# Performance work log

Hardware: AMD Instinct MI355X
Metric: run time of the kernel (lower is better)

Reference implementation:

```python
import jax, jax.numpy as jnp
import numpy as np

B, C, N = 2, 1024, 80
D = 3 * C + 2  # 3074 token dim
DFF = 2048     # torch TransformerEncoderLayer default dim_feedforward
HW = 224
REFINE = 3
EPS = 1e-5


def _layernorm(x, g, b):
    m = jnp.mean(x, axis=-1, keepdims=True)
    v = jnp.mean((x - m) ** 2, axis=-1, keepdims=True)
    return g * (x - m) / jnp.sqrt(v + EPS) + b


def _pos_encoding(seq_len, dim):
    pos = jnp.arange(seq_len, dtype=jnp.float32)[:, None]
    div = jnp.exp(jnp.arange(0, dim, 2, dtype=jnp.float32) * (-np.log(10000.0) / dim))
    pe = jnp.zeros((seq_len, dim), dtype=jnp.float32)
    pe = pe.at[:, 0::2].set(jnp.sin(pos * div)).at[:, 1::2].set(jnp.cos(pos * div))
    return pe


def _forward(pre_f, curr_f, first_f, ln_g, ln_b, ipw, ipb, opw, opb,
             n1g, n1b, l1w, l1b, l2w, l2b, n2g, n2b, ow, ob,
             prev_b, first_b):
    # --- vectorized find_best_shift: batched circular L1 correlation ---
    idx = (jnp.arange(N)[None, :] - jnp.arange(N)[:, None]) % N  # [shift, pos]
    rolled = first_b[:, idx]                                     # [B, N, N, 2]
    dist = jnp.abs(prev_b[:, None] - rolled).sum(axis=(-1, -2))  # [B, N]
    best = jnp.argmin(dist, axis=1)                              # first min, like torch loop
    roll_idx = (jnp.arange(N)[None, :] - best[:, None]) % N      # [B, N]
    first_b = jax.vmap(lambda fb, ri: fb[ri])(first_b, roll_idx)

    # --- bilinear upsample to 224x224 (F.interpolate, align_corners=False) ---
    up = lambda f: jax.image.resize(f, (f.shape[0], f.shape[1], HW, HW), method='bilinear')
    pre_up, curr_up, first_up = up(pre_f), up(curr_f), up(first_f)

    # --- vectorized get_bou_features: [B,N,C] gather ---
    gather = jax.vmap(lambda f, b: f[:, b[:, 0], b[:, 1]].T)
    pre_q = gather(pre_up, prev_b)      # [B, N, C]
    first_q = gather(first_up, first_b)  # [B, N, C]

    pe = _pos_encoding(N, D)
    curr = prev_b.astype(jnp.float32)
    scale = 1.0 / jnp.sqrt(jnp.float32(D))
    results = []
    for _ in range(REFINE):
        bf = gather(curr_up, curr.astype(jnp.int32))          # [B, N, C]
        tokens = jnp.concatenate([pre_q, bf, curr, first_q], axis=-1)  # [B, N, D]
        tokens = _layernorm(tokens, ln_g, ln_b)
        tokens = tokens + pe[None]
        # --- TransformerEncoderLayer (post-norm, nhead=1, relu, eval/no dropout) ---
        qkv = tokens @ ipw.T + ipb
        q, k, v = jnp.split(qkv, 3, axis=-1)
        attn = jax.nn.softmax(jnp.einsum('bqd,bkd->bqk', q, k) * scale, axis=-1)
        a = jnp.einsum('bqk,bkd->bqd', attn, v) @ opw.T + opb
        x = _layernorm(tokens + a, n1g, n1b)
        ff = jax.nn.relu(x @ l1w.T + l1b) @ l2w.T + l2b
        x = _layernorm(x + ff, n2g, n2b)
        out = x @ ow.T + ob                                   # [B, N, 1026]
        curr = jnp.clip(curr + out[..., C:], 0.0, 223.0)
        pre_q = pre_q + out[..., :C]
        results.append(curr)
    return jnp.stack(results)  # [REFINE, B, N, 2]


def setup_inputs() -> dict:
    key = jax.random.key(0)
    ks = jax.random.split(key, 12)
    f = lambda i, s: jax.random.normal(ks[i], s, dtype=jnp.float32)
    w = lambda i, s: 0.02 * jax.random.normal(ks[i], s, dtype=jnp.float32)
    return {
        'pre_img_features': f(0, (B, C, 14, 14)),
        'curr_img_features': f(1, (B, C, 14, 14)),
        'first_img_features': f(2, (B, C, 14, 14)),
        'previous_boundary': jax.random.randint(ks[3], (B, N, 2), 0, HW),
        'first_boundary': jax.random.randint(ks[4], (B, N, 2), 0, HW),
        'ln_g': jnp.ones((D,), jnp.float32), 'ln_b': jnp.zeros((D,), jnp.float32),
        'in_proj_w': w(5, (3 * D, D)), 'in_proj_b': jnp.zeros((3 * D,), jnp.float32),
        'out_proj_w': w(6, (D, D)), 'out_proj_b': jnp.zeros((D,), jnp.float32),
        'norm1_g': jnp.ones((D,), jnp.float32), 'norm1_b': jnp.zeros((D,), jnp.float32),
        'lin1_w': w(7, (DFF, D)), 'lin1_b': jnp.zeros((DFF,), jnp.float32),
        'lin2_w': w(8, (D, DFF)), 'lin2_b': jnp.zeros((D,), jnp.float32),
        'norm2_g': jnp.ones((D,), jnp.float32), 'norm2_b': jnp.zeros((D,), jnp.float32),
        'out_w': w(9, (C + 2, D)), 'out_b': jnp.zeros((C + 2,), jnp.float32),
    }


def reference(pre_img_features, curr_img_features, first_img_features,
              previous_boundary, first_boundary,
              ln_g, ln_b, in_proj_w, in_proj_b, out_proj_w, out_proj_b,
              norm1_g, norm1_b, lin1_w, lin1_b, lin2_w, lin2_b,
              norm2_g, norm2_b, out_w, out_b):
    return _forward(pre_img_features, curr_img_features, first_img_features,
                    ln_g, ln_b, in_proj_w, in_proj_b, out_proj_w, out_proj_b,
                    norm1_g, norm1_b, lin1_w, lin1_b, lin2_w, lin2_b,
                    norm2_g, norm2_b, out_w, out_b,
                    previous_boundary, first_boundary)
```

## Files before the change

### kernel.cpp

```cpp
#include <hip/hip_runtime.h>
#include <math.h>

#define B_    2
#define C_    1024
#define N_    80
#define D_    3074
#define DFF_  2048
#define OD_   1026
#define QKV_  9222
#define M_    160
#define EPS_  1e-5f
#define KPD_  3104

typedef __attribute__((ext_vector_type(8))) short bf16x8;
typedef __attribute__((ext_vector_type(4))) float f32x4;

__device__ inline short f2bf(float f) {
    unsigned u = __float_as_uint(f);
    u += 0x7fffu + ((u >> 16) & 1u);
    return (short)(u >> 16);
}

__device__ inline float wave_sum(float v) {
#pragma unroll
    for (int off = 32; off > 0; off >>= 1) v += __shfl_down(v, off, 64);
    return v;
}

__device__ inline float wave_max(float v) {
#pragma unroll
    for (int off = 32; off > 0; off >>= 1) v = fmaxf(v, __shfl_down(v, off, 64));
    return v;
}

__device__ inline void block_reduce_2(float& s, float& s2, float* red) {
    int tid = threadIdx.x;
    int lane = tid & 63, wid = tid >> 6;
    s = wave_sum(s);
    s2 = wave_sum(s2);
    if (lane == 0) { red[wid] = s; red[4 + wid] = s2; }
    __syncthreads();
    if (tid == 0) {
        red[8] = red[0] + red[1] + red[2] + red[3];
        red[9] = red[4] + red[5] + red[6] + red[7];
    }
    __syncthreads();
    s = red[8]; s2 = red[9];
}

__device__ inline void bilin_setup(int p, int& i0, int& i1, float& t) {
    float s = (p + 0.5f) * 0.0625f - 0.5f;
    s = fminf(fmaxf(s, 0.0f), 13.0f);
    i0 = (int)s;
    t = s - (float)i0;
    i1 = min(i0 + 1, 13);
}

__device__ inline float bilin_tap(const float* f, int y0, int y1, float ty,
                                  int x0, int x1, float tx) {
    float a = f[y0 * 14 + x0], b = f[y0 * 14 + x1];
    float c = f[y1 * 14 + x0], d = f[y1 * 14 + x1];
    return (1.f - ty) * ((1.f - tx) * a + tx * b) + ty * ((1.f - tx) * c + tx * d);
}

__global__ __launch_bounds__(128) void align_kernel(const int* __restrict__ prev_b,
                                                    const int* __restrict__ first_b,
                                                    int* __restrict__ fb_al) {
    int b = blockIdx.x;
    int tid = threadIdx.x;
    __shared__ int dist[N_];
    __shared__ int bestIdx;
    if (tid < N_) {
        int s = 0;
        for (int j = 0; j < N_; ++j) {
            int src = (j - tid) % N_;
            if (src < 0) src += N_;
            int dy = prev_b[(b * N_ + j) * 2] - first_b[(b * N_ + src) * 2];
            int dx = prev_b[(b * N_ + j) * 2 + 1] - first_b[(b * N_ + src) * 2 + 1];
            s += abs(dy) + abs(dx);
        }
        dist[tid] = s;
    }
    __syncthreads();
    if (tid == 0) {
        int best = 0, bd = dist[0];
        for (int i = 1; i < N_; ++i)
            if (dist[i] < bd) { bd = dist[i]; best = i; }
        bestIdx = best;
    }
    __syncthreads();
    if (tid < N_) {
        int src = (tid - bestIdx) % N_;
        if (src < 0) src += N_;
        fb_al[(b * N_ + tid) * 2]     = first_b[(b * N_ + src) * 2];
        fb_al[(b * N_ + tid) * 2 + 1] = first_b[(b * N_ + src) * 2 + 1];
    }
}

__global__ __launch_bounds__(256) void gather_init_kernel(
        const float* __restrict__ pre_f, const float* __restrict__ first_f,
        const int* __restrict__ prev_b, const int* __restrict__ fb_al,
        float* __restrict__ pre_q, float* __restrict__ first_q,
        float* __restrict__ curr) {
    int m = blockIdx.x;
    int b = m / N_;
    int tid = threadIdx.x;
    int py = prev_b[m * 2], px = prev_b[m * 2 + 1];
    int fy = fb_al[m * 2], fx = fb_al[m * 2 + 1];
    int py0, py1, px0, px1, fy0, fy1, fx0, fx1;
    float pty, ptx, fty, ftx;
    bilin_setup(py, py0, py1, pty);
    bilin_setup(px, px0, px1, ptx);
    bilin_setup(fy, fy0, fy1, fty);
    bilin_setup(fx, fx0, fx1, ftx);
    for (int c = tid; c < C_; c += 256) {
        const float* fp = pre_f + (size_t)(b * C_ + c) * 196;
        const float* ff = first_f + (size_t)(b * C_ + c) * 196;
        pre_q[(size_t)m * C_ + c]   = bilin_tap(fp, py0, py1, pty, px0, px1, ptx);
        first_q[(size_t)m * C_ + c] = bilin_tap(ff, fy0, fy1, fty, fx0, fx1, ftx);
    }
    if (tid < 2) curr[m * 2 + tid] = (float)prev_b[m * 2 + tid];
}

__global__ __launch_bounds__(256) void tokens_kernel(
        const float* __restrict__ curr_f, const float* __restrict__ pre_q,
        const float* __restrict__ first_q, const float* __restrict__ curr,
        const float* __restrict__ ln_g, const float* __restrict__ ln_b,
        float* __restrict__ tokens, short* __restrict__ tokens_bf) {
    int m = blockIdx.x;
    int b = m / N_;
    int n = m % N_;
    int tid = threadIdx.x;
    __shared__ float bf[C_];
    __shared__ float red[10];

    float cy = curr[m * 2], cx = curr[m * 2 + 1];
    int iy = (int)cy, ix = (int)cx;
    int y0, y1, x0, x1;
    float ty, tx;
    bilin_setup(iy, y0, y1, ty);
    bilin_setup(ix, x0, x1, tx);
    for (int c = tid; c < C_; c += 256) {
        const float* f = curr_f + (size_t)(b * C_ + c) * 196;
        bf[c] = bilin_tap(f, y0, y1, ty, x0, x1, tx);
    }
    __syncthreads();

    float s = 0.f, s2 = 0.f;
    for (int d = tid; d < D_; d += 256) {
        float v;
        if (d < C_)            v = pre_q[(size_t)m * C_ + d];
        else if (d < 2 * C_)   v = bf[d - C_];
        else if (d == 2 * C_)  v = cy;
        else if (d == 2*C_+1)  v = cx;
        else                   v = first_q[(size_t)m * C_ + (d - 2 * C_ - 2)];
        s += v; s2 += v * v;
    }
    block_reduce_2(s, s2, red);
    float mean = s / (float)D_;
    float var = s2 / (float)D_ - mean * mean;
    float inv = rsqrtf(var + EPS_);

    const float negLogDivD = -logf(10000.0f) / (float)D_;
    for (int d = tid; d < KPD_; d += 256) {
        if (d < D_) {
            float v;
            if (d < C_)            v = pre_q[(size_t)m * C_ + d];
            else if (d < 2 * C_)   v = bf[d - C_];
            else if (d == 2 * C_)  v = cy;
            else if (d == 2*C_+1)  v = cx;
            else                   v = first_q[(size_t)m * C_ + (d - 2 * C_ - 2)];
            float ln = ln_g[d] * (v - mean) * inv + ln_b[d];
            int kk = d >> 1;
            float ang = (float)n * expf((float)(2 * kk) * negLogDivD);
            float pe = (d & 1) ? cosf(ang) : sinf(ang);
            float val = ln + pe;
            tokens[(size_t)m * D_ + d] = val;
            tokens_bf[(size_t)m * KPD_ + d] = f2bf(val);
        } else {
            tokens_bf[(size_t)m * KPD_ + d] = 0;
        }
    }
}

__global__ __launch_bounds__(256) void wpack_kernel(const float* __restrict__ w,
                                                    short* __restrict__ o,
                                                    int K, int O, int nch) {
    int s = blockIdx.x;
    int items = nch * 64;
    for (int idx = threadIdx.x; idx < items; idx += 256) {
        int c = idx >> 6, l = idx & 63;
        int col = l & 15, quad = l >> 4;
        int orow = s * 16 + col;
        int k0 = c * 32 + quad * 8;
        bf16x8 v;
        if (orow < O && k0 + 8 <= K) {
            const float* src = w + (size_t)orow * K + k0;
            float2 a = *(const float2*)(src);
            float2 b = *(const float2*)(src + 2);
            float2 cc = *(const float2*)(src + 4);
            float2 d = *(const float2*)(src + 6);
            v[0] = f2bf(a.x);  v[1] = f2bf(a.y);
            v[2] = f2bf(b.x);  v[3] = f2bf(b.y);
            v[4] = f2bf(cc.x); v[5] = f2bf(cc.y);
            v[6] = f2bf(d.x);  v[7] = f2bf(d.y);
        } else {
#pragma unroll
            for (int j = 0; j < 8; ++j) {
                int k = k0 + j;
                v[j] = (orow < O && k < K) ? f2bf(w[(size_t)orow * K + k]) : (short)0;
            }
        }
        *(bf16x8*)(o + ((size_t)s * nch + c) * 512 + l * 8) = v;
    }
}

__global__ __launch_bounds__(256) void gemm_pk(
        const short* __restrict__ A, const short* __restrict__ Wp,
        const float* __restrict__ bias, float* __restrict__ Cout,
        int KpA, int nch, int O) {
    int strip = blockIdx.x;
    int nsk = gridDim.y;
    int mg = blockIdx.z;
    int lane = threadIdx.x & 63, wave = threadIdx.x >> 6;
    int col = lane & 15, quad = lane >> 4;

    int per = (nch + nsk - 1) / nsk;
    int cs = blockIdx.y * per;
    int ce = min(nch, cs + per);
    if (cs >= ce) return;
    int tot = ce - cs;
    int qn = tot >> 2, rmd = tot & 3;
    int c0 = cs + wave * qn + min(wave, rmd);
    int c1 = c0 + qn + (wave < rmd ? 1 : 0);

    const short* wp = Wp + (size_t)strip * nch * 512 + lane * 8;
    const short* ap = A + (size_t)(mg * 80 + col) * KpA + quad * 8;

    f32x4 acc[5];
#pragma unroll
    for (int t = 0; t < 5; ++t)
#pragma unroll
        for (int r = 0; r < 4; ++r) acc[t][r] = 0.f;

    if (c0 < c1) {
        bf16x8 wcur = *(const bf16x8*)(wp + (size_t)c0 * 512);
        for (int c = c0; c < c1; ++c) {
            bf16x8 wnxt = wcur;
            if (c + 1 < c1) wnxt = *(const bf16x8*)(wp + (size_t)(c + 1) * 512);
#pragma unroll
            for (int t = 0; t < 5; ++t) {
                bf16x8 af = *(const bf16x8*)(ap + (size_t)t * 16 * KpA + c * 32);
                acc[t] = __builtin_amdgcn_mfma_f32_16x16x32_bf16(af, wcur, acc[t], 0, 0, 0);
            }
            wcur = wnxt;
        }
    }

    __shared__ f32x4 red[4][5][64];
#pragma unroll
    for (int t = 0; t < 5; ++t) red[wave][t][lane] = acc[t];
    __syncthreads();
    for (int item = threadIdx.x; item < 320; item += 256) {
        int t = item >> 6, l2 = item & 63;
        f32x4 v = red[0][t][l2];
#pragma unroll
        for (int w = 1; w < 4; ++w)
#pragma unroll
            for (int r = 0; r < 4; ++r) v[r] += red[w][t][l2][r];
        int oc = strip * 16 + (l2 & 15);
        if (oc < O) {
            float bv = (blockIdx.y == 0) ? bias[oc] : 0.f;
            int rbase = mg * 80 + t * 16 + (l2 >> 4) * 4;
#pragma unroll
            for (int r = 0; r < 4; ++r) {
                float val = v[r] + bv;
                if (nsk == 1) Cout[(size_t)(rbase + r) * O + oc] = val;
                else atomicAdd(&Cout[(size_t)(rbase + r) * O + oc], val);
            }
        }
    }
}

__global__ __launch_bounds__(256) void gemm_mfma_sk(
        const short* __restrict__ A, const float* __restrict__ Wf,
        const float* __restrict__ bias, float* __restrict__ Cout,
        int K, int KpA, int O, int KC) {
    int kc0 = blockIdx.y * KC;
    if (kc0 >= K) return;
    int kend = min(K, kc0 + KC);

    int lane = threadIdx.x & 63;
    int wave = threadIdx.x >> 6;
    int col  = lane & 15;
    int quad = lane >> 4;
    int o0 = blockIdx.x * 128 + wave * 32 + col;
    int o1 = o0 + 16;
    int oc0 = min(o0, O - 1), oc1 = min(o1, O - 1);

    const float* wrow0 = Wf + (size_t)oc0 * K + quad * 8;
    const float* wrow1 = Wf + (size_t)oc1 * K + quad * 8;
    const short* abase = A + (size_t)col * KpA + quad * 8;

    f32x4 acc0[10], acc1[10];
#pragma unroll
    for (int t = 0; t < 10; ++t)
#pragma unroll
        for (int r = 0; r < 4; ++r) { acc0[t][r] = 0.f; acc1[t][r] = 0.f; }

    int nfull = (kend - kc0) >> 5;
    bf16x8 aCur[10];
    float2 wCur[8];
    if (nfull > 0) {
#pragma unroll
        for (int t = 0; t < 10; ++t)
            aCur[t] = *(const bf16x8*)(abase + (size_t)t * 16 * KpA + kc0);
#pragma unroll
        for (int j = 0; j < 4; ++j) {
            wCur[j]     = *(const float2*)(wrow0 + kc0 + 2 * j);
            wCur[4 + j] = *(const float2*)(wrow1 + kc0 + 2 * j);
        }
    }
    for (int i = 0; i < nfull; ++i) {
        bf16x8 aNxt[10];
        float2 wNxt[8];
        if (i + 1 < nfull) {
            int kn = kc0 + (i + 1) * 32;
#pragma unroll
            for (int t = 0; t < 10; ++t)
                aNxt[t] = *(const bf16x8*)(abase + (size_t)t * 16 * KpA + kn);
#pragma unroll
            for (int j = 0; j < 4; ++j) {
                wNxt[j]     = *(const float2*)(wrow0 + kn + 2 * j);
                wNxt[4 + j] = *(const float2*)(wrow1 + kn + 2 * j);
            }
        }
        bf16x8 b0, b1;
#pragma unroll
        for (int j = 0; j < 4; ++j) {
            b0[2*j] = f2bf(wCur[j].x);     b0[2*j+1] = f2bf(wCur[j].y);
            b1[2*j] = f2bf(wCur[4+j].x);   b1[2*j+1] = f2bf(wCur[4+j].y);
        }
#pragma unroll
        for (int t = 0; t < 10; ++t) {
            acc0[t] = __builtin_amdgcn_mfma_f32_16x16x32_bf16(aCur[t], b0, acc0[t], 0, 0, 0);
            acc1[t] = __builtin_amdgcn_mfma_f32_16x16x32_bf16(aCur[t], b1, acc1[t], 0, 0, 0);
        }
#pragma unroll
        for (int t = 0; t < 10; ++t) aCur[t] = aNxt[t];
#pragma unroll
        for (int j = 0; j < 8; ++j) wCur[j] = wNxt[j];
    }
    int kmain = kc0 + nfull * 32;
    if (kmain < kend) {
        bf16x8 b0, b1;
#pragma unroll
        for (int j = 0; j < 8; ++j) {
            int k = kmain + quad * 8 + j;
            b0[j] = (k < kend) ? f2bf(Wf[(size_t)oc0 * K + k]) : (short)0;
            b1[j] = (k < kend) ? f2bf(Wf[(size_t)oc1 * K + k]) : (short)0;
        }
#pragma unroll
        for (int t = 0; t < 10; ++t) {
            bf16x8 af = *(const bf16x8*)(abase + (size_t)t * 16 * KpA + kmain);
            acc0[t] = __builtin_amdgcn_mfma_f32_16x16x32_bf16(af, b0, acc0[t], 0, 0, 0);
            acc1[t] = __builtin_amdgcn_mfma_f32_16x16x32_bf16(af, b1, acc1[t], 0, 0, 0);
        }
    }
    if (o0 < O) {
        float bv = (blockIdx.y == 0) ? bias[o0] : 0.f;
#pragma unroll
        for (int t = 0; t < 10; ++t)
#pragma unroll
            for (int r = 0; r < 4; ++r)
                atomicAdd(&Cout[(size_t)(t * 16 + quad * 4 + r) * O + o0], acc0[t][r] + bv);
    }
    if (o1 < O) {
        float bv = (blockIdx.y == 0) ? bias[o1] : 0.f;
#pragma unroll
        for (int t = 0; t < 10; ++t)
#pragma unroll
            for (int r = 0; r < 4; ++r)
                atomicAdd(&Cout[(size_t)(t * 16 + quad * 4 + r) * O + o1], acc1[t][r] + bv);
    }
}

__global__ __launch_bounds__(256) void relu_cvt_kernel(const float* __restrict__ in,
                                                       short* __restrict__ out,
                                                       int n) {
    int i = blockIdx.x * 256 + threadIdx.x;
    if (i < n) out[i] = f2bf(fmaxf(in[i], 0.f));
}

__global__ __launch_bounds__(256) void qkv_cvt_kernel(const float* __restrict__ qkv,
                                                      short* __restrict__ q_bf,
                                                      short* __restrict__ k_bf,
                                                      short* __restrict__ v_bf) {
    int m = blockIdx.x;
    int b = m / N_, q = m % N_;
    const float* src = qkv + (size_t)m * QKV_;
    for (int d = threadIdx.x; d < KPD_; d += 256) {
        short qv = (d < D_) ? f2bf(src[d])          : (short)0;
        short kv = (d < D_) ? f2bf(src[D_ + d])     : (short)0;
        short vv = (d < D_) ? f2bf(src[2 * D_ + d]) : (short)0;
        q_bf[(size_t)m * KPD_ + d] = qv;
        k_bf[(size_t)m * KPD_ + d] = kv;
        v_bf[((size_t)b * 96 + q) * KPD_ + d] = vv;
    }
}

__global__ __launch_bounds__(256) void scores_mfma(const short* __restrict__ q_bf,
                                                   const short* __restrict__ k_bf,
                                                   float* __restrict__ sc) {
    int bi = blockIdx.x;
    int b = bi / 25, qt = (bi % 25) / 5, kt = bi % 5;
    int lane = threadIdx.x & 63, wave = threadIdx.x >> 6;
    int col = lane & 15, quad = lane >> 4;
    const short* qbase = q_bf + (size_t)(b * N_ + qt * 16 + col) * KPD_ + quad * 8;
    const short* kbase = k_bf + (size_t)(b * N_ + kt * 16 + col) * KPD_ + quad * 8;
    f32x4 acc;
#pragma unroll
    for (int r = 0; r < 4; ++r) acc[r] = 0.f;
    int c0 = wave * 25, c1 = min(97, c0 + 25);
    for (int c = c0; c < c1; ++c) {
        bf16x8 af = *(const bf16x8*)(qbase + c * 32);
        bf16x8 bf8 = *(const bf16x8*)(kbase + c * 32);
        acc = __builtin_amdgcn_mfma_f32_16x16x32_bf16(af, bf8, acc, 0, 0, 0);
    }
    __shared__ f32x4 red[4][64];
    red[wave][lane] = acc;
    __syncthreads();
    if (threadIdx.x < 64) {
        f32x4 t = red[0][lane];
#pragma unroll
        for (int w = 1; w < 4; ++w)
#pragma unroll
            for (int r = 0; r < 4; ++r) t[r] += red[w][lane][r];
        float scale = rsqrtf((float)D_);
#pragma unroll
        for (int r = 0; r < 4; ++r)
            sc[(size_t)(b * N_ + qt * 16 + quad * 4 + r) * N_ + kt * 16 + col] = t[r] * scale;
    }
}

__global__ __launch_bounds__(256) void softmax_kernel(const float* __restrict__ sc,
                                                      short* __restrict__ p_bf) {
    int m = blockIdx.x * 4 + (threadIdx.x >> 6);
    int lane = threadIdx.x & 63;
    const float* row = sc + (size_t)m * N_;
    float a = row[lane];
    float bv = (lane < 16) ? row[64 + lane] : -1e30f;
    float mx = wave_max(fmaxf(a, bv));
    mx = __shfl(mx, 0, 64);
    float e0 = expf(a - mx);
    float e1 = (lane < 16) ? expf(bv - mx) : 0.f;
    float sum = wave_sum(e0 + e1);
    sum = __shfl(sum, 0, 64);
    float rs = 1.0f / sum;
    p_bf[(size_t)m * 96 + lane] = f2bf(e0 * rs);
    if (lane < 32)
        p_bf[(size_t)m * 96 + 64 + lane] = (lane < 16) ? f2bf(e1 * rs) : (short)0;
}

__global__ __launch_bounds__(256) void av_mfma(const short* __restrict__ p_bf,
                                               const short* __restrict__ v_bf,
                                               short* __restrict__ av_bf) {
    int bi = blockIdx.x;
    int b = bi / 49, g = bi % 49;
    int lane = threadIdx.x & 63, wave = threadIdx.x >> 6;
    int dtile = g * 4 + wave;
    if (dtile >= 194) return;
    int d0 = dtile * 16;
    int col = lane & 15, quad = lane >> 4;
    const short* pbase = p_bf + (size_t)b * N_ * 96 + quad * 8;
    const short* vb = v_bf + (size_t)b * 96 * KPD_ + d0 + col;
    f32x4 acc[5];
#pragma unroll
    for (int t = 0; t < 5; ++t)
#pragma unroll
        for (int r = 0; r < 4; ++r) acc[t][r] = 0.f;
#pragma unroll
    for (int c = 0; c < 3; ++c) {
        bf16x8 bf8;
#pragma unroll
        for (int j = 0; j < 8; ++j)
            bf8[j] = vb[(size_t)(c * 32 + quad * 8 + j) * KPD_];
#pragma unroll
        for (int t = 0; t < 5; ++t) {
            bf16x8 af = *(const bf16x8*)(pbase + (size_t)(t * 16 + col) * 96 + c * 32);
            acc[t] = __builtin_amdgcn_mfma_f32_16x16x32_bf16(af, bf8, acc[t], 0, 0, 0);
        }
    }
#pragma unroll
    for (int t = 0; t < 5; ++t)
#pragma unroll
        for (int r = 0; r < 4; ++r)
            av_bf[(size_t)(b * N_ + t * 16 + quad * 4 + r) * KPD_ + d0 + col] = f2bf(acc[t][r]);
}

template <bool WF32>
__global__ __launch_bounds__(256) void ln_kernel(const float* __restrict__ xin,
                                                 const float* __restrict__ res,
                                                 const float* __restrict__ g,
                                                 const float* __restrict__ bta,
                                                 float* __restrict__ outf,
                                                 short* __restrict__ outb) {
    int m = blockIdx.x;
    int tid = threadIdx.x;
    __shared__ float red[10];
    const float* xr = xin + (size_t)m * D_;
    const float* rr = res + (size_t)m * D_;
    float s = 0.f, s2 = 0.f;
    for (int d = tid; d < D_; d += 256) {
        float v = xr[d] + rr[d];
        s += v; s2 += v * v;
    }
    block_reduce_2(s, s2, red);
    float mean = s / (float)D_;
    float var = s2 / (float)D_ - mean * mean;
    float inv = rsqrtf(var + EPS_);
    for (int d = tid; d < KPD_; d += 256) {
        if (d < D_) {
            float v = xr[d] + rr[d];
            float y = g[d] * (v - mean) * inv + bta[d];
            if (WF32) outf[(size_t)m * D_ + d] = y;
            outb[(size_t)m * KPD_ + d] = f2bf(y);
        } else {
            outb[(size_t)m * KPD_ + d] = 0;
        }
    }
}

__global__ __launch_bounds__(256) void update_kernel(const float* __restrict__ outb,
                                                     float* __restrict__ curr,
                                                     float* __restrict__ pre_q,
                                                     float* __restrict__ results) {
    int m = blockIdx.x;
    int tid = threadIdx.x;
    for (int c = tid; c < C_; c += 256)
        pre_q[(size_t)m * C_ + c] += outb[(size_t)m * OD_ + c];
    if (tid < 2) {
        float nc = curr[m * 2 + tid] + outb[(size_t)m * OD_ + C_ + tid];
        nc = fminf(fmaxf(nc, 0.f), 223.f);
        curr[m * 2 + tid] = nc;
        results[m * 2 + tid] = nc;
    }
}

extern "C" void kernel_launch(void* const* d_in, const int* in_sizes, int n_in,
                              void* d_out, int out_size, void* d_ws, size_t ws_size,
                              hipStream_t stream) {
    const float* pre_f   = (const float*)d_in[0];
    const float* curr_f  = (const float*)d_in[1];
    const float* first_f = (const float*)d_in[2];
    const int*   prev_b  = (const int*)d_in[3];
    const int*   first_b = (const int*)d_in[4];
    const float* ln_g    = (const float*)d_in[5];
    const float* ln_b    = (const float*)d_in[6];
    const float* ipw     = (const float*)d_in[7];
    const float* ipb     = (const float*)d_in[8];
    const float* opw     = (const float*)d_in[9];
    const float* opb     = (const float*)d_in[10];
    const float* n1g     = (const float*)d_in[11];
    const float* n1b     = (const float*)d_in[12];
    const float* l1w     = (const float*)d_in[13];
    const float* l1b     = (const float*)d_in[14];
    const float* l2w     = (const float*)d_in[15];
    const float* l2b     = (const float*)d_in[16];
    const float* n2g     = (const float*)d_in[17];
    const float* n2b     = (const float*)d_in[18];
    const float* ow      = (const float*)d_in[19];
    const float* ob      = (const float*)d_in[20];
    float* outp = (float*)d_out;

    float* wf = (float*)d_ws;
    size_t off = 0;
    int*   fb_al   = (int*)(wf + off); off += 320;
    float* curr    = wf + off;         off += 320;
    float* pre_q   = wf + off;         off += (size_t)M_ * C_;
    float* first_q = wf + off;         off += (size_t)M_ * C_;
    float* tokens  = wf + off;         off += (size_t)M_ * D_;
    float* qkv     = wf + off;         off += (size_t)M_ * QKV_;
    float* aout    = wf + off;         off += (size_t)M_ * D_;
    float* xbuf    = wf + off;         off += (size_t)M_ * D_;
    float* ff1f    = wf + off;         off += (size_t)M_ * DFF_;
    float* ffout   = wf + off;         off += (size_t)M_ * D_;
    float* outb    = wf + off;         off += (size_t)M_ * OD_;
    float* sc      = wf + off;         off += (size_t)M_ * N_;
    short* tokens_bf = (short*)(wf + off); off += (size_t)M_ * KPD_ / 2;
    short* x_bf      = (short*)(wf + off); off += (size_t)M_ * KPD_ / 2;
    short* x2_bf     = (short*)(wf + off); off += (size_t)M_ * KPD_ / 2;
    short* av_bf     = (short*)(wf + off); off += (size_t)M_ * KPD_ / 2;
    short* ff1_bf    = (short*)(wf + off); off += (size_t)M_ * DFF_ / 2;
    short* q_bf      = (short*)(wf + off); off += (size_t)M_ * KPD_ / 2;
    short* k_bf      = (short*)(wf + off); off += (size_t)M_ * KPD_ / 2;
    short* v_bf      = (short*)(wf + off); off += (size_t)B_ * 96 * KPD_ / 2;
    short* p_bf      = (short*)(wf + off); off += (size_t)M_ * 96 / 2;
    short* ipw_pk = (short*)(wf + off); off += (size_t)577 * 97 * 256;
    short* opw_pk = (short*)(wf + off); off += (size_t)193 * 97 * 256;
    short* l1w_pk = (short*)(wf + off); off += (size_t)128 * 97 * 256;
    short* l2w_pk = (short*)(wf + off); off += (size_t)193 * 64 * 256;
    short* ow_pk  = (short*)(wf + off); off += (size_t)65  * 97 * 256;
    bool use_bf = ws_size >= off * sizeof(float);
    (void)in_sizes; (void)n_in; (void)out_size;

    hipLaunchKernelGGL(align_kernel, dim3(B_), dim3(128), 0, stream,
                       prev_b, first_b, fb_al);
    hipLaunchKernelGGL(gather_init_kernel, dim3(M_), dim3(256), 0, stream,
                       pre_f, first_f, prev_b, fb_al, pre_q, first_q, curr);
    hipMemsetAsync(v_bf, 0, (size_t)B_ * 96 * KPD_ * 2, stream);

    if (use_bf) {
        hipLaunchKernelGGL(wpack_kernel, dim3(577), dim3(256), 0, stream, ipw, ipw_pk, D_, QKV_, 97);
        hipLaunchKernelGGL(wpack_kernel, dim3(193), dim3(256), 0, stream, opw, opw_pk, D_, D_, 97);
        hipLaunchKernelGGL(wpack_kernel, dim3(128), dim3(256), 0, stream, l1w, l1w_pk, D_, DFF_, 97);
        hipLaunchKernelGGL(wpack_kernel, dim3(193), dim3(256), 0, stream, l2w, l2w_pk, DFF_, D_, 64);
        hipLaunchKernelGGL(wpack_kernel, dim3(65),  dim3(256), 0, stream, ow, ow_pk, D_, OD_, 97);
    }

    for (int it = 0; it < 3; ++it) {
        if (!use_bf) hipMemsetAsync(qkv, 0, (size_t)M_ * QKV_ * 4, stream);
        hipMemsetAsync(aout,  0, (size_t)M_ * D_   * 4, stream);
        hipMemsetAsync(ff1f,  0, (size_t)M_ * DFF_ * 4, stream);
        hipMemsetAsync(ffout, 0, (size_t)M_ * D_   * 4, stream);
        hipMemsetAsync(outb,  0, (size_t)M_ * OD_  * 4, stream);

        hipLaunchKernelGGL(tokens_kernel, dim3(M_), dim3(256), 0, stream,
                           curr_f, pre_q, first_q, curr, ln_g, ln_b, tokens, tokens_bf);
        if (use_bf)
            hipLaunchKernelGGL(gemm_pk, dim3(577, 1, 2), dim3(256), 0, stream,
                               tokens_bf, ipw_pk, ipb, qkv, KPD_, 97, QKV_);
        else
            hipLaunchKernelGGL(gemm_mfma_sk, dim3(73, 6), dim3(256), 0, stream,
                               tokens_bf, ipw, ipb, qkv, D_, KPD_, QKV_, 544);
        hipLaunchKernelGGL(qkv_cvt_kernel, dim3(M_), dim3(256), 0, stream,
                           qkv, q_bf, k_bf, v_bf);
        hipLaunchKernelGGL(scores_mfma, dim3(50), dim3(256), 0, stream,
                           q_bf, k_bf, sc);
        hipLaunchKernelGGL(softmax_kernel, dim3(40), dim3(256), 0, stream,
                           sc, p_bf);
        hipLaunchKernelGGL(av_mfma, dim3(98), dim3(256), 0, stream,
                           p_bf, v_bf, av_bf);
        if (use_bf)
            hipLaunchKernelGGL(gemm_pk, dim3(193, 2, 2), dim3(256), 0, stream,
                               av_bf, opw_pk, opb, aout, KPD_, 97, D_);
        else
            hipLaunchKernelGGL(gemm_mfma_sk, dim3(25, 10), dim3(256), 0, stream,
                               av_bf, opw, opb, aout, D_, KPD_, D_, 320);
        hipLaunchKernelGGL((ln_kernel<true>), dim3(M_), dim3(256), 0, stream,
                           tokens, aout, n1g, n1b, xbuf, x_bf);
        if (use_bf)
            hipLaunchKernelGGL(gemm_pk, dim3(128, 2, 2), dim3(256), 0, stream,
                               x_bf, l1w_pk, l1b, ff1f, KPD_, 97, DFF_);
        else
            hipLaunchKernelGGL(gemm_mfma_sk, dim3(16, 17), dim3(256), 0, stream,
                               x_bf, l1w, l1b, ff1f, D_, KPD_, DFF_, 192);
        hipLaunchKernelGGL(relu_cvt_kernel, dim3((M_ * DFF_ + 255) / 256), dim3(256), 0, stream,
                           ff1f, ff1_bf, M_ * DFF_);
        if (use_bf)
            hipLaunchKernelGGL(gemm_pk, dim3(193, 2, 2), dim3(256), 0, stream,
                               ff1_bf, l2w_pk, l2b, ffout, DFF_, 64, D_);
        else
            hipLaunchKernelGGL(gemm_mfma_sk, dim3(25, 11), dim3(256), 0, stream,
                               ff1_bf, l2w, l2b, ffout, DFF_, DFF_, D_, 192);
        hipLaunchKernelGGL((ln_kernel<false>), dim3(M_), dim3(256), 0, stream,
                           xbuf, ffout, n2g, n2b, (float*)nullptr, x2_bf);
        if (use_bf)
            hipLaunchKernelGGL(gemm_pk, dim3(65, 4, 2), dim3(256), 0, stream,
                               x2_bf, ow_pk, ob, outb, KPD_, 97, OD_);
        else
            hipLaunchKernelGGL(gemm_mfma_sk, dim3(9, 13), dim3(256), 0, stream,
                               x2_bf, ow, ob, outb, D_, KPD_, OD_, 256);
        hipLaunchKernelGGL(update_kernel, dim3(M_), dim3(256), 0, stream,
                           outb, curr, pre_q, outp + (size_t)it * M_ * 2);
    }
}
```

Measured before the change: 1.040 ms.

## Add split-K LDS double-buffered GEMM writing partials, reduce them in consumer kernels

Adds a gemm_stage kernel that stages the 160-row activation tile in LDS with double buffering and gives each wave several output strips. Each split-K slice writes plain stores into a partial buffer instead of using atomics. The downstream kernels (qkv_cvt, ln, relu_cvt, update) now sum those partials, so the per-iteration memsets and atomic traffic go away. Weight packing is also spread over more blocks. The cost is a large partial buffer and extra read traffic in the reduction kernels, and the new path only runs when the workspace is big enough.

After: 1.134 ms. +9.0%, slower.

```diff
diff --git a/kernel.cpp b/kernel.cpp
--- a/kernel.cpp
+++ b/kernel.cpp
@@ -11,6 +11,12 @@
 #define M_    160
 #define EPS_  1e-5f
 #define KPD_  3104
+
+#define SQKV 6
+#define SOP  14
+#define SFF1 14
+#define SFF2 16
+#define SHD  14
 
 typedef __attribute__((ext_vector_type(8))) short bf16x8;
 typedef __attribute__((ext_vector_type(4))) float f32x4;
@@ -188,7 +194,10 @@
                                                     int K, int O, int nch) {
     int s = blockIdx.x;
     int items = nch * 64;
-    for (int idx = threadIdx.x; idx < items; idx += 256) {
+    int qlen = (items + 3) >> 2;
+    int beg = blockIdx.y * qlen;
+    int end = min(items, beg + qlen);
+    for (int idx = beg + threadIdx.x; idx < end; idx += 256) {
         int c = idx >> 6, l = idx & 63;
         int col = l & 15, quad = l >> 4;
         int orow = s * 16 + col;
@@ -215,6 +224,98 @@
     }
 }
 
+template <int SW>
+__global__ __launch_bounds__(256) void gemm_stage(
+        const short* __restrict__ A, const short* __restrict__ Wp,
+        const float* __restrict__ bias, float* __restrict__ part,
+        int KpA, int nch, int O, int per) {
+    int cs = blockIdx.y * per;
+    int ce = min(nch, cs + per);
+    if (cs >= ce) return;
+    int tid = threadIdx.x;
+    int lane = tid & 63, wave = tid >> 6;
+    int col = lane & 15, quad = lane >> 4;
+    int s0 = (blockIdx.x * 4 + wave) * SW;
+
+    __shared__ short lbuf[2][160 * 32];
+
+    int m0 = tid >> 2, p8 = (tid & 3) * 8;
+    int m1 = (tid + 256) >> 2;
+    int m2 = (tid + 512) >> 2;
+    const short* a0 = A + (size_t)m0 * KpA + p8;
+    const short* a1 = A + (size_t)m1 * KpA + p8;
+    const short* a2 = A + (size_t)m2 * KpA + p8;
+    bf16x8 sr0, sr1, sr2;
+
+    f32x4 acc[SW][10];
+#pragma unroll
+    for (int j = 0; j < SW; ++j)
+#pragma unroll
+        for (int t = 0; t < 10; ++t)
+#pragma unroll
+            for (int r = 0; r < 4; ++r) acc[j][t][r] = 0.f;
+
+    const short* wbase[SW];
+#pragma unroll
+    for (int j = 0; j < SW; ++j)
+        wbase[j] = Wp + (size_t)(s0 + j) * nch * 512 + lane * 8;
+    bf16x8 wc[SW], wn[SW];
+
+    sr0 = *(const bf16x8*)(a0 + cs * 32);
+    sr1 = *(const bf16x8*)(a1 + cs * 32);
+    if (tid < 128) sr2 = *(const bf16x8*)(a2 + cs * 32);
+#pragma unroll
+    for (int j = 0; j < SW; ++j)
+        wc[j] = *(const bf16x8*)(wbase[j] + (size_t)cs * 512);
+    *(bf16x8*)(&lbuf[0][m0 * 32 + p8]) = sr0;
+    *(bf16x8*)(&lbuf[0][m1 * 32 + p8]) = sr1;
+    if (tid < 128) *(bf16x8*)(&lbuf[0][m2 * 32 + p8]) = sr2;
+    __syncthreads();
+
+    int cur = 0;
+    for (int c = cs; c < ce; ++c) {
+        bool more = (c + 1) < ce;
+        if (more) {
+            sr0 = *(const bf16x8*)(a0 + (c + 1) * 32);
+            sr1 = *(const bf16x8*)(a1 + (c + 1) * 32);
+            if (tid < 128) sr2 = *(const bf16x8*)(a2 + (c + 1) * 32);
+#pragma unroll
+            for (int j = 0; j < SW; ++j)
+                wn[j] = *(const bf16x8*)(wbase[j] + (size_t)(c + 1) * 512);
+        }
+#pragma unroll
+        for (int t = 0; t < 10; ++t) {
+            bf16x8 af = *(const bf16x8*)(&lbuf[cur][t * 512 + col * 32 + quad * 8]);
+#pragma unroll
+            for (int j = 0; j < SW; ++j)
+                acc[j][t] = __builtin_amdgcn_mfma_f32_16x16x32_bf16(af, wc[j], acc[j][t], 0, 0, 0);
+        }
+        if (more) {
+            *(bf16x8*)(&lbuf[cur ^ 1][m0 * 32 + p8]) = sr0;
+            *(bf16x8*)(&lbuf[cur ^ 1][m1 * 32 + p8]) = sr1;
+            if (tid < 128) *(bf16x8*)(&lbuf[cur ^ 1][m2 * 32 + p8]) = sr2;
+        }
+        __syncthreads();
+#pragma unroll
+        for (int j = 0; j < SW; ++j) wc[j] = wn[j];
+        cur ^= 1;
+    }
+
+    float* pout = part + (size_t)blockIdx.y * M_ * O;
+#pragma unroll
+    for (int j = 0; j < SW; ++j) {
+        int oc = (s0 + j) * 16 + col;
+        if (oc < O) {
+            float bv = (blockIdx.y == 0) ? bias[oc] : 0.f;
+#pragma unroll
+            for (int t = 0; t < 10; ++t)
+#pragma unroll
+                for (int r = 0; r < 4; ++r)
+                    pout[(size_t)(t * 16 + quad * 4 + r) * O + oc] = acc[j][t][r] + bv;
+        }
+    }
+}
+
 __global__ __launch_bounds__(256) void gemm_pk(
         const short* __restrict__ A, const short* __restrict__ Wp,
         const float* __restrict__ bias, float* __restrict__ Cout,
@@ -386,23 +487,34 @@
 }
 
 __global__ __launch_bounds__(256) void relu_cvt_kernel(const float* __restrict__ in,
+                                                       int S, size_t sstr,
                                                        short* __restrict__ out,
                                                        int n) {
     int i = blockIdx.x * 256 + threadIdx.x;
-    if (i < n) out[i] = f2bf(fmaxf(in[i], 0.f));
-}
-
-__global__ __launch_bounds__(256) void qkv_cvt_kernel(const float* __restrict__ qkv,
+    if (i < n) {
+        float v = 0.f;
+        for (int s = 0; s < S; ++s) v += in[(size_t)s * sstr + i];
+        out[i] = f2bf(fmaxf(v, 0.f));
+    }
+}
+
+__global__ __launch_bounds__(256) void qkv_cvt_kernel(const float* __restrict__ part,
+                                                      int S,
                                                       short* __restrict__ q_bf,
                                                       short* __restrict__ k_bf,
                                                       short* __restrict__ v_bf) {
     int m = blockIdx.x;
     int b = m / N_, q = m % N_;
-    const float* src = qkv + (size_t)m * QKV_;
     for (int d = threadIdx.x; d < KPD_; d += 256) {
-        short qv = (d < D_) ? f2bf(src[d])          : (short)0;
-        short kv = (d < D_) ? f2bf(src[D_ + d])     : (short)0;
-        short vv = (d < D_) ? f2bf(src[2 * D_ + d]) : (short)0;
+        short qv = 0, kv = 0, vv = 0;
+        if (d < D_) {
+            float qf = 0.f, kf = 0.f, vf = 0.f;
+            for (int s = 0; s < S; ++s) {
+                const float* p = part + (size_t)s * M_ * QKV_ + (size_t)m * QKV_;
+                qf += p[d]; kf += p[D_ + d]; vf += p[2 * D_ + d];
+            }
+            qv = f2bf(qf); kv = f2bf(kf); vv = f2bf(vf);
+        }
         q_bf[(size_t)m * KPD_ + d] = qv;
         k_bf[(size_t)m * KPD_ + d] = kv;
         v_bf[((size_t)b * 96 + q) * KPD_ + d] = vv;
@@ -500,6 +612,7 @@
 
 template <bool WF32>
 __global__ __launch_bounds__(256) void ln_kernel(const float* __restrict__ xin,
+                                                 int S, size_t sstr,
                                                  const float* __restrict__ res,
                                                  const float* __restrict__ g,
                                                  const float* __restrict__ bta,
@@ -510,37 +623,53 @@
     __shared__ float red[10];
     const float* xr = xin + (size_t)m * D_;
     const float* rr = res + (size_t)m * D_;
+    float vv[13];
     float s = 0.f, s2 = 0.f;
-    for (int d = tid; d < D_; d += 256) {
-        float v = xr[d] + rr[d];
-        s += v; s2 += v * v;
+#pragma unroll
+    for (int i = 0; i < 13; ++i) {
+        int d = tid + i * 256;
+        float v = 0.f;
+        if (d < D_) {
+            v = rr[d];
+            for (int sp = 0; sp < S; ++sp) v += xr[(size_t)sp * sstr + d];
+            s += v; s2 += v * v;
+        }
+        vv[i] = v;
     }
     block_reduce_2(s, s2, red);
     float mean = s / (float)D_;
     float var = s2 / (float)D_ - mean * mean;
     float inv = rsqrtf(var + EPS_);
-    for (int d = tid; d < KPD_; d += 256) {
+#pragma unroll
+    for (int i = 0; i < 13; ++i) {
+        int d = tid + i * 256;
         if (d < D_) {
-            float v = xr[d] + rr[d];
-            float y = g[d] * (v - mean) * inv + bta[d];
+            float y = g[d] * (vv[i] - mean) * inv + bta[d];
             if (WF32) outf[(size_t)m * D_ + d] = y;
             outb[(size_t)m * KPD_ + d] = f2bf(y);
-        } else {
+        } else if (d < KPD_) {
             outb[(size_t)m * KPD_ + d] = 0;
         }
     }
 }
 
-__global__ __launch_bounds__(256) void update_kernel(const float* __restrict__ outb,
+__global__ __launch_bounds__(256) void update_kernel(const float* __restrict__ part,
+                                                     int S, size_t sstr,
                                                      float* __restrict__ curr,
                                                      float* __restrict__ pre_q,
                                                      float* __restrict__ results) {
     int m = blockIdx.x;
     int tid = threadIdx.x;
-    for (int c = tid; c < C_; c += 256)
-        pre_q[(size_t)m * C_ + c] += outb[(size_t)m * OD_ + c];
+    const float* pr = part + (size_t)m * OD_;
+    for (int c = tid; c < C_; c += 256) {
+        float v = 0.f;
+        for (int s = 0; s < S; ++s) v += pr[(size_t)s * sstr + c];
+        pre_q[(size_t)m * C_ + c] += v;
+    }
     if (tid < 2) {
-        float nc = curr[m * 2 + tid] + outb[(size_t)m * OD_ + C_ + tid];
+        float v = 0.f;
+        for (int s = 0; s < S; ++s) v += pr[(size_t)s * sstr + C_ + tid];
+        float nc = curr[m * 2 + tid] + v;
         nc = fminf(fmaxf(nc, 0.f), 223.f);
         curr[m * 2 + tid] = nc;
         results[m * 2 + tid] = nc;
@@ -580,12 +709,7 @@
     float* pre_q   = wf + off;         off += (size_t)M_ * C_;
     float* first_q = wf + off;         off += (size_t)M_ * C_;
     float* tokens  = wf + off;         off += (size_t)M_ * D_;
-    float* qkv     = wf + off;         off += (size_t)M_ * QKV_;
-    float* aout    = wf + off;         off += (size_t)M_ * D_;
     float* xbuf    = wf + off;         off += (size_t)M_ * D_;
-    float* ff1f    = wf + off;         off += (size_t)M_ * DFF_;
-    float* ffout   = wf + off;         off += (size_t)M_ * D_;
-    float* outb    = wf + off;         off += (size_t)M_ * OD_;
     float* sc      = wf + off;         off += (size_t)M_ * N_;
     short* tokens_bf = (short*)(wf + off); off += (size_t)M_ * KPD_ / 2;
     short* x_bf      = (short*)(wf + off); off += (size_t)M_ * KPD_ / 2;
@@ -596,13 +720,33 @@
     short* k_bf      = (short*)(wf + off); off += (size_t)M_ * KPD_ / 2;
     short* v_bf      = (short*)(wf + off); off += (size_t)B_ * 96 * KPD_ / 2;
     short* p_bf      = (short*)(wf + off); off += (size_t)M_ * 96 / 2;
-    short* ipw_pk = (short*)(wf + off); off += (size_t)577 * 97 * 256;
-    short* opw_pk = (short*)(wf + off); off += (size_t)193 * 97 * 256;
-    short* l1w_pk = (short*)(wf + off); off += (size_t)128 * 97 * 256;
-    short* l2w_pk = (short*)(wf + off); off += (size_t)193 * 64 * 256;
-    short* ow_pk  = (short*)(wf + off); off += (size_t)65  * 97 * 256;
-    bool use_bf = ws_size >= off * sizeof(float);
-    (void)in_sizes; (void)n_in; (void)out_size;
+    size_t commonF = off;
+
+    size_t o2 = commonF;
+    short* ipw_p2 = (short*)(wf + o2); o2 += (size_t)584 * 97 * 256;
+    short* opw_p2 = (short*)(wf + o2); o2 += (size_t)200 * 97 * 256;
+    short* l1w_p2 = (short*)(wf + o2); o2 += (size_t)128 * 97 * 256;
+    short* l2w_p2 = (short*)(wf + o2); o2 += (size_t)200 * 64 * 256;
+    short* ow_p2  = (short*)(wf + o2); o2 += (size_t)68  * 97 * 256;
+    float* gpart  = wf + o2;           o2 += (size_t)SQKV * M_ * QKV_;
+
+    size_t o1 = commonF;
+    float* qkv   = wf + o1; o1 += (size_t)M_ * QKV_;
+    float* aout  = wf + o1; o1 += (size_t)M_ * D_;
+    float* ff1f  = wf + o1; o1 += (size_t)M_ * DFF_;
+    float* ffout = wf + o1; o1 += (size_t)M_ * D_;
+    float* outb  = wf + o1; o1 += (size_t)M_ * OD_;
+    size_t o0 = o1;
+    short* ipw_p1 = (short*)(wf + o1); o1 += (size_t)577 * 97 * 256;
+    short* opw_p1 = (short*)(wf + o1); o1 += (size_t)193 * 97 * 256;
+    short* l1w_p1 = (short*)(wf + o1); o1 += (size_t)128 * 97 * 256;
+    short* l2w_p1 = (short*)(wf + o1); o1 += (size_t)193 * 64 * 256;
+    short* ow_p1  = (short*)(wf + o1); o1 += (size_t)65  * 97 * 256;
+
+    int tier = (ws_size >= o2 * sizeof(float)) ? 2
+             : (ws_size >= o1 * sizeof(float)) ? 1
+             : 0;
+    (void)in_sizes; (void)n_in; (void)out_size; (void)o0;
 
     hipLaunchKernelGGL(align_kernel, dim3(B_), dim3(128), 0, stream,
                        prev_b, first_b, fb_al);
@@ -610,68 +754,96 @@
                        pre_f, first_f, prev_b, fb_al, pre_q, first_q, curr);
     hipMemsetAsync(v_bf, 0, (size_t)B_ * 96 * KPD_ * 2, stream);
 
-    if (use_bf) {
-        hipLaunchKernelGGL(wpack_kernel, dim3(577), dim3(256), 0, stream, ipw, ipw_pk, D_, QKV_, 97);
-        hipLaunchKernelGGL(wpack_kernel, dim3(193), dim3(256), 0, stream, opw, opw_pk, D_, D_, 97);
-        hipLaunchKernelGGL(wpack_kernel, dim3(128), dim3(256), 0, stream, l1w, l1w_pk, D_, DFF_, 97);
-        hipLaunchKernelGGL(wpack_kernel, dim3(193), dim3(256), 0, stream, l2w, l2w_pk, DFF_, D_, 64);
-        hipLaunchKernelGGL(wpack_kernel, dim3(65),  dim3(256), 0, stream, ow, ow_pk, D_, OD_, 97);
+    if (tier == 2) {
+        hipLaunchKernelGGL(wpack_kernel, dim3(584, 4), dim3(256), 0, stream, ipw, ipw_p2, D_, QKV_, 97);
+        hipLaunchKernelGGL(wpack_kernel, dim3(200, 4), dim3(256), 0, stream, opw, opw_p2, D_, D_, 97);
+        hipLaunchKernelGGL(wpack_kernel, dim3(128, 4), dim3(256), 0, stream, l1w, l1w_p2, D_, DFF_, 97);
+        hipLaunchKernelGGL(wpack_kernel, dim3(200, 4), dim3(256), 0, stream, l2w, l2w_p2, DFF_, D_, 64);
+        hipLaunchKernelGGL(wpack_kernel, dim3(68, 4),  dim3(256), 0, stream, ow, ow_p2, D_, OD_, 97);
+    } else if (tier == 1) {
+        hipLaunchKernelGGL(wpack_kernel, dim3(577, 4), dim3(256), 0, stream, ipw, ipw_p1, D_, QKV_, 97);
+        hipLaunchKernelGGL(wpack_kernel, dim3(193, 4), dim3(256), 0, stream, opw, opw_p1, D_, D_, 97);
+        hipLaunchKernelGGL(wpack_kernel, dim3(128, 4), dim3(256), 0, stream, l1w, l1w_p1, D_, DFF_, 97);
+        hipLaunchKernelGGL(wpack_kernel, dim3(193, 4), dim3(256), 0, stream, l2w, l2w_p1, DFF_, D_, 64);
+        hipLaunchKernelGGL(wpack_kernel, dim3(65, 4),  dim3(256), 0, stream, ow, ow_p1, D_, OD_, 97);
     }
 
     for (int it = 0; it < 3; ++it) {
-        if (!use_bf) hipMemsetAsync(qkv, 0, (size_t)M_ * QKV_ * 4, stream);
-        hipMemsetAsync(aout,  0, (size_t)M_ * D_   * 4, stream);
-        hipMemsetAsync(ff1f,  0, (size_t)M_ * DFF_ * 4, stream);
-        hipMemsetAsync(ffout, 0, (size_t)M_ * D_   * 4, stream);
-        hipMemsetAsync(outb,  0, (size_t)M_ * OD_  * 4, stream);
+        if (tier < 2) {
+            if (tier == 0) hipMemsetAsync(qkv, 0, (size_t)M_ * QKV_ * 4, stream);
+            hipMemsetAsync(aout,  0, (size_t)M_ * D_   * 4, stream);
+            hipMemsetAsync(ff1f,  0, (size_t)M_ * DFF_ * 4, stream);
+            hipMemsetAsync(ffout, 0, (size_t)M_ * D_   * 4, stream);
+            hipMemsetAsync(outb,  0, (size_t)M_ * OD_  * 4, stream);
+        }
 
         hipLaunchKernelGGL(tokens_kernel, dim3(M_), dim3(256), 0, stream,
                            curr_f, pre_q, first_q, curr, ln_g, ln_b, tokens, tokens_bf);
-        if (use_bf)
+        if (tier == 2)
+            hipLaunchKernelGGL((gemm_stage<2>), dim3(73, SQKV), dim3(256), 0, stream,
+                               tokens_bf, ipw_p2, ipb, gpart, KPD_, 97, QKV_, (97 + SQKV - 1) / SQKV);
+        else if (tier == 1)
             hipLaunchKernelGGL(gemm_pk, dim3(577, 1, 2), dim3(256), 0, stream,
-                               tokens_bf, ipw_pk, ipb, qkv, KPD_, 97, QKV_);
+                               tokens_bf, ipw_p1, ipb, qkv, KPD_, 97, QKV_);
         else
             hipLaunchKernelGGL(gemm_mfma_sk, dim3(73, 6), dim3(256), 0, stream,
                                tokens_bf, ipw, ipb, qkv, D_, KPD_, QKV_, 544);
         hipLaunchKernelGGL(qkv_cvt_kernel, dim3(M_), dim3(256), 0, stream,
-                           qkv, q_bf, k_bf, v_bf);
+                           (tier == 2) ? gpart : qkv, (tier == 2) ? SQKV : 1,
+                           q_bf, k_bf, v_bf);
         hipLaunchKernelGGL(scores_mfma, dim3(50), dim3(256), 0, stream,
                            q_bf, k_bf, sc);
         hipLaunchKernelGGL(softmax_kernel, dim3(40), dim3(256), 0, stream,
                            sc, p_bf);
         hipLaunchKernelGGL(av_mfma, dim3(98), dim3(256), 0, stream,
                            p_bf, v_bf, av_bf);
-        if (use_bf)
+        if (tier == 2)
+            hipLaunchKernelGGL((gemm_stage<2>), dim3(25, SOP), dim3(256), 0, stream,
+                               av_bf, opw_p2, opb, gpart, KPD_, 97, D_, (97 + SOP - 1) / SOP);
+        else if (tier == 1)
             hipLaunchKernelGGL(gemm_pk, dim3(193, 2, 2), dim3(256), 0, stream,
-                               av_bf, opw_pk, opb, aout, KPD_, 97, D_);
+                               av_bf, opw_p1, opb, aout, KPD_, 97, D_);
         else
             hipLaunchKernelGGL(gemm_mfma_sk, dim3(25, 10), dim3(256), 0, stream,
                                av_bf, opw, opb, aout, D_, KPD_, D_, 320);
         hipLaunchKernelGGL((ln_kernel<true>), dim3(M_), dim3(256), 0, stream,
-                           tokens, aout, n1g, n1b, xbuf, x_bf);
-        if (use_bf)
+                           (tier == 2) ? gpart : aout, (tier == 2) ? SOP : 1, (size_t)M_ * D_,
+                           tokens, n1g, n1b, xbuf, x_bf);
+        if (tier == 2)
+            hipLaunchKernelGGL((gemm_stage<2>), dim3(16, SFF1), dim3(256), 0, stream,
+                               x_bf, l1w_p2, l1b, gpart, KPD_, 97, DFF_, (97 + SFF1 - 1) / SFF1);
+        else if (tier == 1)
             hipLaunchKernelGGL(gemm_pk, dim3(128, 2, 2), dim3(256), 0, stream,
-                               x_bf, l1w_pk, l1b, ff1f, KPD_, 97, DFF_);
+                               x_bf, l1w_p1, l1b, ff1f, KPD_, 97, DFF_);
         else
             hipLaunchKernelGGL(gemm_mfma_sk, dim3(16, 17), dim3(256), 0, stream,
                                x_bf, l1w, l1b, ff1f, D_, KPD_, DFF_, 192);
         hipLaunchKernelGGL(relu_cvt_kernel, dim3((M_ * DFF_ + 255) / 256), dim3(256), 0, stream,
-                           ff1f, ff1_bf, M_ * DFF_);
-        if (use_bf)
+                           (tier == 2) ? gpart : ff1f, (tier == 2) ? SFF1 : 1, (size_t)M_ * DFF_,
+                           ff1_bf, M_ * DFF_);
+        if (tier == 2)
+            hipLaunchKernelGGL((gemm_stage<2>), dim3(25, SFF2), dim3(256), 0, stream,
+                               ff1_bf, l2w_p2, l2b, gpart, DFF_, 64, D_, (64 + SFF2 - 1) / SFF2);
+        else if (tier == 1)
             hipLaunchKernelGGL(gemm_pk, dim3(193, 2, 2), dim3(256), 0, stream,
-                               ff1_bf, l2w_pk, l2b, ffout, DFF_, 64, D_);
+                               ff1_bf, l2w_p1, l2b, ffout, DFF_, 64, D_);
         else
             hipLaunchKernelGGL(gemm_mfma_sk, dim3(25, 11), dim3(256), 0, stream,
                                ff1_bf, l2w, l2b, ffout, DFF_, DFF_, D_, 192);
         hipLaunchKernelGGL((ln_kernel<false>), dim3(M_), dim3(256), 0, stream,
-                           xbuf, ffout, n2g, n2b, (float*)nullptr, x2_bf);
-        if (use_bf)
+                           (tier == 2) ? gpart : ffout, (tier == 2) ? SFF2 : 1, (size_t)M_ * D_,
+                           xbuf, n2g, n2b, (float*)nullptr, x2_bf);
+        if (tier == 2)
+            hipLaunchKernelGGL((gemm_stage<1>), dim3(17, SHD), dim3(256), 0, stream,
+                               x2_bf, ow_p2, ob, gpart, KPD_, 97, OD_, (97 + SHD - 1) / SHD);
+        else if (tier == 1)
             hipLaunchKernelGGL(gemm_pk, dim3(65, 4, 2), dim3(256), 0, stream,
-                               x2_bf, ow_pk, ob, outb, KPD_, 97, OD_);
+                               x2_bf, ow_p1, ob, outb, KPD_, 97, OD_);
         else
             hipLaunchKernelGGL(gemm_mfma_sk, dim3(9, 13), dim3(256), 0, stream,
                                x2_bf, ow, ob, outb, D_, KPD_, OD_, 256);
         hipLaunchKernelGGL(update_kernel, dim3(M_), dim3(256), 0, stream,
-                           outb, curr, pre_q, outp + (size_t)it * M_ * 2);
-    }
-}
+                           (tier == 2) ? gpart : outb, (tier == 2) ? SHD : 1, (size_t)M_ * OD_,
+                           curr, pre_q, outp + (size_t)it * M_ * 2);
+    }
+}
```
